# Optimization experiments

Hardware: AMD Instinct MI355X
Metric: run time of the kernel (lower is better)

## Reference

```python
import jax, jax.numpy as jnp
import numpy as np

N_NODES = 50000
N_EDGES = 800000
N_GRAPHS = 16
F_IN = 128
E_DIM = 16
HID = 32
HEADS = 2
EPS_BN = 1e-5


def gatv2_conv(x, edge_index, edge_attr, Wl, bl, Wr, br, We, att, bias, heads, out_ch):
    """PyG GATv2Conv (share_weights=False, concat=True, add_self_loops=True, fill_value='mean')."""
    n = x.shape[0]
    src, dst = edge_index[0], edge_index[1]
    loop = jnp.arange(n)
    src = jnp.concatenate([src, loop])
    dst = jnp.concatenate([dst, loop])
    ea = jnp.concatenate([edge_attr, jnp.broadcast_to(edge_attr.mean(0), (n, edge_attr.shape[1]))])
    x_l = (x @ Wl + bl).reshape(n, heads, out_ch)   # source transform
    x_r = (x @ Wr + br).reshape(n, heads, out_ch)   # target transform
    e = (ea @ We).reshape(-1, heads, out_ch)
    m = jax.nn.leaky_relu(x_l[src] + x_r[dst] + e, 0.2)      # [E, H, C]
    alpha = (m * att[None]).sum(-1)                          # [E, H]
    amax = jax.ops.segment_max(alpha, dst, num_segments=n)
    ex = jnp.exp(alpha - amax[dst])
    denom = jax.ops.segment_sum(ex, dst, num_segments=n)
    alpha = ex / (denom[dst] + 1e-16)
    out = jax.ops.segment_sum(x_l[src] * alpha[..., None], dst, num_segments=n)
    return out.reshape(n, heads * out_ch) + bias


def batch_norm(x, g, b):
    mu = x.mean(0)
    var = jnp.var(x, axis=0)  # biased, as torch BatchNorm1d training mode
    return (x - mu) * jax.lax.rsqrt(var + EPS_BN) * g + b


def setup_inputs() -> dict:
    key = jax.random.key(0)
    ks = jax.random.split(key, 24)
    s = 0.1
    d1 = HID * HEADS  # 64
    inp = {
        'x': jax.random.normal(ks[0], (N_NODES, F_IN), jnp.float32),
        'edge_index': jax.random.randint(ks[1], (2, N_EDGES), 0, N_NODES),
        'edge_attr': jax.random.normal(ks[2], (N_EDGES, E_DIM), jnp.float32),
        'batch': jnp.sort(jax.random.randint(ks[3], (N_NODES,), 0, N_GRAPHS)),
        'skip1_W': jax.random.normal(ks[4], (F_IN, d1)) * s,
        'skip1_b': jnp.zeros((d1,)),
        'conv1_Wl': jax.random.normal(ks[5], (F_IN, d1)) * s,
        'conv1_bl': jnp.zeros((d1,)),
        'conv1_Wr': jax.random.normal(ks[6], (F_IN, d1)) * s,
        'conv1_br': jnp.zeros((d1,)),
        'conv1_We': jax.random.normal(ks[7], (E_DIM, d1)) * s,
        'conv1_att': jax.random.normal(ks[8], (HEADS, HID)) * s,
        'conv1_bias': jnp.zeros((d1,)),
        'bn1_g': jnp.ones((d1,)),
        'bn1_b': jnp.zeros((d1,)),
        'skip2_W': jax.random.normal(ks[9], (d1, HID)) * s,
        'skip2_b': jnp.zeros((HID,)),
        'conv2_Wl': jax.random.normal(ks[10], (d1, HID)) * s,
        'conv2_bl': jnp.zeros((HID,)),
        'conv2_Wr': jax.random.normal(ks[11], (d1, HID)) * s,
        'conv2_br': jnp.zeros((HID,)),
        'conv2_We': jax.random.normal(ks[12], (E_DIM, HID)) * s,
        'conv2_att': jax.random.normal(ks[13], (1, HID)) * s,
        'conv2_bias': jnp.zeros((HID,)),
        'bn2_g': jnp.ones((HID,)),
        'bn2_b': jnp.zeros((HID,)),
    }
    return inp


def reference(x, edge_index, edge_attr, batch,
              skip1_W, skip1_b, conv1_Wl, conv1_bl, conv1_Wr, conv1_br, conv1_We, conv1_att, conv1_bias, bn1_g, bn1_b,
              skip2_W, skip2_b, conv2_Wl, conv2_bl, conv2_Wr, conv2_br, conv2_We, conv2_att, conv2_bias, bn2_g, bn2_b):
    h_proj = x @ skip1_W + skip1_b
    h = gatv2_conv(x, edge_index, edge_attr, conv1_Wl, conv1_bl, conv1_Wr, conv1_br, conv1_We, conv1_att, conv1_bias, HEADS, HID)
    h = jax.nn.elu(batch_norm(h, bn1_g, bn1_b) + h_proj)
    h_proj = h @ skip2_W + skip2_b
    h2 = gatv2_conv(h, edge_index, edge_attr, conv2_Wl, conv2_bl, conv2_Wr, conv2_br, conv2_We, conv2_att, conv2_bias, 1, HID)
    h2 = jax.nn.elu(batch_norm(h2, bn2_g, bn2_b) + h_proj)
    ones = jnp.ones((h2.shape[0],), h2.dtype)
    counts = jax.ops.segment_sum(ones, batch, num_segments=N_GRAPHS)
    x_mean = jax.ops.segment_sum(h2, batch, num_segments=N_GRAPHS) / jnp.maximum(counts, 1.0)[:, None]
    x_max = jax.ops.segment_max(h2, batch, num_segments=N_GRAPHS)
    x_max = jnp.where(counts[:, None] > 0, x_max, 0.0)
    return jnp.concatenate([x_mean, x_max], axis=1)
```

## Files before the change

kernel.cpp:

```cpp
#include <hip/hip_runtime.h>
#include <hip/hip_bf16.h>

#define NE 800000
#define NN 50000
#define NG 16
#define ETOT (NE + NN)

typedef unsigned short u16;
typedef __attribute__((ext_vector_type(8))) short short8;
typedef __attribute__((ext_vector_type(4))) float float4v;

__device__ __forceinline__ float b2f(u16 u) {
  return __uint_as_float(((unsigned)u) << 16);
}
__device__ __forceinline__ u16 f2b(float f) {
  __hip_bfloat16 b = __float2bfloat16(f);
  return *(u16*)&b;
}
__device__ __forceinline__ void cv8(uint4 v, float* o) {
  o[0] = __uint_as_float(v.x << 16);
  o[1] = __uint_as_float(v.x & 0xFFFF0000u);
  o[2] = __uint_as_float(v.y << 16);
  o[3] = __uint_as_float(v.y & 0xFFFF0000u);
  o[4] = __uint_as_float(v.z << 16);
  o[5] = __uint_as_float(v.z & 0xFFFF0000u);
  o[6] = __uint_as_float(v.w << 16);
  o[7] = __uint_as_float(v.w & 0xFFFF0000u);
}
__device__ __forceinline__ unsigned pk2(float a, float b) {
  return (unsigned)f2b(a) | ((unsigned)f2b(b) << 16);
}
__device__ __forceinline__ unsigned f2key(float f) {
  unsigned u = __float_as_uint(f);
  return (u & 0x80000000u) ? ~u : (u | 0x80000000u);
}
__device__ __forceinline__ float key2f(unsigned k) {
  unsigned u = (k & 0x80000000u) ? (k ^ 0x80000000u) : ~k;
  return __uint_as_float(u);
}
__device__ __forceinline__ int plaus(unsigned h) {
  unsigned eh = (h >> 7) & 0xFF;
  return (h == 0) || (eh >= 100 && eh <= 140);
}
__device__ __forceinline__ float lrelu(float v) {
  return (v > 0.f) ? v : 0.2f * v;
}

__global__ __launch_bounds__(256) void k_init(uint4* __restrict__ zbase, int zcnt16,
                                              const unsigned* __restrict__ a,
                                              const unsigned* __restrict__ b,
                                              const unsigned* __restrict__ c,
                                              int* __restrict__ flags) {
  uint4 z = {0, 0, 0, 0};
  for (int i = blockIdx.x * 256 + threadIdx.x; i < zcnt16; i += gridDim.x * 256)
    zbase[i] = z;
  if (blockIdx.x != 0) return;
  __shared__ int cnt[3];
  if (threadIdx.x < 3) cnt[threadIdx.x] = 0;
  __syncthreads();
  const unsigned* arr[3] = {a, b, c};
  for (int k = 0; k < 3; k++) {
    int ok = 0;
    for (int i = threadIdx.x; i < 4096; i += 256) {
      unsigned w = arr[k][i];
      ok += (plaus(w & 0xFFFFu) && plaus(w >> 16)) ? 1 : 0;
    }
    atomicAdd(&cnt[k], ok);
  }
  __syncthreads();
  if (threadIdx.x == 0) {
    int f0 = cnt[0] > 2048, f1 = cnt[1] > 2048, f2 = cnt[2] > 2048;
    flags[0] = f0;
    flags[1] = f1;
    flags[2] = f2;
    flags[3] = f0 && f1 && f2;
  }
}

__global__ __launch_bounds__(256) void k_histcol(const int* __restrict__ ei,
                                                 const void* __restrict__ ea,
                                                 const int* __restrict__ flg,
                                                 int* __restrict__ deg,
                                                 float* __restrict__ sums) {
  int gt = blockIdx.x * 256 + threadIdx.x;
  if (gt < ETOT) {
    int dst = (gt < NE) ? ei[NE + gt] : gt - NE;
    atomicAdd(&deg[dst], 1);
  }
  bool eb = flg[2] != 0;
  int col = gt & 15;
  int row = gt >> 4;
  int rstride = (gridDim.x * 256) >> 4;
  float s = 0.f;
  if (eb) {
    const u16* p = (const u16*)ea;
    for (int e = row; e < NE; e += rstride) s += b2f(p[(size_t)e * 16 + col]);
  } else {
    const float* p = (const float*)ea;
    for (int e = row; e < NE; e += rstride) s += p[(size_t)e * 16 + col];
  }
  __shared__ float ls[256];
  ls[threadIdx.x] = s;
  __syncthreads();
  if (threadIdx.x < 16) {
    float t = 0.f;
    for (int i = threadIdx.x; i < 256; i += 16) t += ls[i];
    atomicAdd(&sums[threadIdx.x], t);
  }
}

template <int K, int N>
__device__ __forceinline__ void load_W_f32(float* Wf, const void* W, bool wb) {
  if (wb) {
    const u16* Wp = (const u16*)W;
    for (int i = threadIdx.x; i < K * N / 8; i += 256) {
      float t[8];
      cv8(*(const uint4*)(Wp + i * 8), t);
#pragma unroll
      for (int q = 0; q < 8; q++) Wf[i * 8 + q] = t[q];
    }
  } else {
    const float* Wp = (const float*)W;
    for (int i = threadIdx.x; i < K * N / 4; i += 256) {
      float4 v = *(const float4*)(Wp + i * 4);
      Wf[i * 4 + 0] = v.x; Wf[i * 4 + 1] = v.y;
      Wf[i * 4 + 2] = v.z; Wf[i * 4 + 3] = v.w;
    }
  }
}

template <int K, int N, int RPB>
__device__ __forceinline__ void gemm_mfma_tile(
    const float* __restrict__ Wf,
    const void* __restrict__ xin, bool xb, bool wb,
    const void* __restrict__ bb, u16* __restrict__ out, int tile) {
  constexpr int CT = N / 16;
  constexpr int WPC = 4 / CT;
  constexpr int KK = K / 32;
  int lane = threadIdx.x & 63;
  int wave = threadIdx.x >> 6;
  int col = lane & 15;
  int quad = lane >> 4;
  int ct = wave % CT;
  int rt_off = wave / CT;
  short8 bh[KK], bl[KK];
#pragma unroll
  for (int kk = 0; kk < KK; kk++) {
    short8 th, tl;
#pragma unroll
    for (int j = 0; j < 8; j++) {
      float w = Wf[(kk * 32 + quad * 8 + j) * N + ct * 16 + col];
      u16 hb = f2b(w);
      th[j] = (short)hb;
      tl[j] = (short)f2b(w - b2f(hb));
    }
    bh[kk] = th;
    bl[kk] = tl;
  }
  float bias = wb ? b2f(((const u16*)bb)[ct * 16 + col])
                  : ((const float*)bb)[ct * 16 + col];
  int rt0 = tile * RPB;
  for (int i = rt_off; i < RPB; i += WPC) {
    int rt = rt0 + i;
    int row = rt * 16 + col;
    float4v acc = {0.f, 0.f, 0.f, 0.f};
    if (xb) {
      const u16* xp = (const u16*)xin;
#pragma unroll
      for (int kk = 0; kk < KK; kk++) {
        short8 af = *(const short8*)(xp + (size_t)row * K + kk * 32 + quad * 8);
        acc = __builtin_amdgcn_mfma_f32_16x16x32_bf16(af, bh[kk], acc, 0, 0, 0);
        if (!wb)
          acc = __builtin_amdgcn_mfma_f32_16x16x32_bf16(af, bl[kk], acc, 0, 0, 0);
      }
    } else {
      const float* xp = (const float*)xin;
#pragma unroll
      for (int kk = 0; kk < KK; kk++) {
        float4 v0 = *(const float4*)(xp + (size_t)row * K + kk * 32 + quad * 8);
        float4 v1 = *(const float4*)(xp + (size_t)row * K + kk * 32 + quad * 8 + 4);
        float a[8] = {v0.x, v0.y, v0.z, v0.w, v1.x, v1.y, v1.z, v1.w};
        short8 ah, al;
#pragma unroll
        for (int j = 0; j < 8; j++) {
          u16 hb = f2b(a[j]);
          ah[j] = (short)hb;
          al[j] = (short)f2b(a[j] - b2f(hb));
        }
        acc = __builtin_amdgcn_mfma_f32_16x16x32_bf16(ah, bh[kk], acc, 0, 0, 0);
        acc = __builtin_amdgcn_mfma_f32_16x16x32_bf16(al, bh[kk], acc, 0, 0, 0);
        if (!wb)
          acc = __builtin_amdgcn_mfma_f32_16x16x32_bf16(ah, bl[kk], acc, 0, 0, 0);
      }
    }
#pragma unroll
    for (int r = 0; r < 4; r++) {
      int orow = rt * 16 + quad * 4 + r;
      out[(size_t)orow * N + ct * 16 + col] = f2b(acc[r] + bias);
    }
  }
}

template <int K, int N, int TILES, int RPB>
__global__ __launch_bounds__(256) void k_scanlin1(
    const int* __restrict__ deg, int* __restrict__ start, int* __restrict__ cursor,
    const void* __restrict__ xin, const int* __restrict__ flg,
    const void* W0, const void* W1, const void* W2,
    const void* b0, const void* b1, const void* b2,
    u16* __restrict__ o0, u16* __restrict__ o1, u16* __restrict__ o2, int M) {
  (void)M;
  __shared__ __align__(16) float smem[K * N];

  if ((int)blockIdx.x == 3 * TILES) {
    int* wsum = (int*)smem;
    int t = threadIdx.x;
    int lane = t & 63;
    int wv = t >> 6;
    int carry = 0;
    for (int base = 0; base < NN; base += 1024) {
      int idx = base + t * 4;
      int4 d = {0, 0, 0, 0};
      if (idx + 3 < NN) {
        d = *(const int4*)(deg + idx);
      } else {
        if (idx + 0 < NN) d.x = deg[idx + 0];
        if (idx + 1 < NN) d.y = deg[idx + 1];
        if (idx + 2 < NN) d.z = deg[idx + 2];
        if (idx + 3 < NN) d.w = deg[idx + 3];
      }
      int s4 = d.x + d.y + d.z + d.w;
      int sc = s4;
#pragma unroll
      for (int ofs = 1; ofs < 64; ofs <<= 1) {
        int v = __shfl_up(sc, ofs, 64);
        if (lane >= ofs) sc += v;
      }
      if (lane == 63) wsum[wv] = sc;
      __syncthreads();
      int wbase = 0;
#pragma unroll
      for (int w = 0; w < 4; w++) {
        int ws = wsum[w];
        if (w < wv) wbase += ws;
      }
      int tile_total = wsum[0] + wsum[1] + wsum[2] + wsum[3];
      __syncthreads();
      int excl = carry + wbase + (sc - s4);
      int4 st;
      st.x = excl;
      st.y = excl + d.x;
      st.z = st.y + d.y;
      st.w = st.z + d.z;
      if (idx + 3 < NN) {
        *(int4*)(start + idx) = st;
        *(int4*)(cursor + idx) = st;
      } else {
        if (idx + 0 < NN) { start[idx + 0] = st.x; cursor[idx + 0] = st.x; }
        if (idx + 1 < NN) { start[idx + 1] = st.y; cursor[idx + 1] = st.y; }
        if (idx + 2 < NN) { start[idx + 2] = st.z; cursor[idx + 2] = st.z; }
        if (idx + 3 < NN) { start[idx + 3] = st.w; cursor[idx + 3] = st.w; }
      }
      carry += tile_total;
    }
    if (t == 0) start[NN] = carry;
    return;
  }
  int lidx = blockIdx.x;
  int wset = lidx / TILES;
  int tile = lidx % TILES;
  bool wb = flg[1] != 0;
  bool xb = flg[0] != 0;
  const void* W = wset == 0 ? W0 : (wset == 1 ? W1 : W2);
  const void* bb = wset == 0 ? b0 : (wset == 1 ? b1 : b2);
  u16* out = wset == 0 ? o0 : (wset == 1 ? o1 : o2);
  load_W_f32<K, N>(smem, W, wb);
  __syncthreads();
  gemm_mfma_tile<K, N, RPB>(smem, xin, xb, wb, bb, out, tile);
}

__global__ __launch_bounds__(256) void k_buildcsr_pay(
    const int* __restrict__ ei, const void* __restrict__ eattr,
    const int* __restrict__ flg, const float* __restrict__ mean_sums,
    int* __restrict__ cursor, int* __restrict__ csr_src,
    u16* __restrict__ ea16) {
  int e = blockIdx.x * 256 + threadIdx.x;
  if (e >= ETOT) return;
  bool eb = flg[2] != 0;
  int src, dst;
  if (e < NE) { src = ei[e]; dst = ei[NE + e]; } else { src = dst = e - NE; }
  float rec[16];
  if (e < NE) {
    if (eb) {
      const uint4* q = (const uint4*)((const u16*)eattr + (size_t)e * 16);
      cv8(q[0], rec);
      cv8(q[1], rec + 8);
    } else {
      const float* q = (const float*)eattr + (size_t)e * 16;
#pragma unroll
      for (int k = 0; k < 16; k++) rec[k] = q[k];
    }
  } else {
#pragma unroll
    for (int k = 0; k < 16; k++) rec[k] = mean_sums[k] * (1.0f / NE);
  }
  int pos = atomicAdd(&cursor[dst], 1);
  csr_src[pos] = src;
  u16 rb[16];
#pragma unroll
  for (int k = 0; k < 16; k++) rb[k] = f2b(rec[k]);
  uint4* dp = (uint4*)(ea16 + (size_t)pos * 16);
  dp[0] = *(uint4*)rb;
  dp[1] = *(uint4*)(rb + 8);
}

__global__ __launch_bounds__(256) void k_buildcsr(const int* __restrict__ ei,
                                                  int* __restrict__ cursor,
                                                  uint2* __restrict__ csr) {
  int e = blockIdx.x * 256 + threadIdx.x;
  if (e >= ETOT) return;
  int src, dst;
  if (e < NE) { src = ei[e]; dst = ei[NE + e]; } else { src = dst = e - NE; }
  int pos = atomicAdd(&cursor[dst], 1);
  uint2 r; r.x = (unsigned)src; r.y = (unsigned)e;
  csr[pos] = r;
}

template <int K, int N, int RPB>
__global__ __launch_bounds__(256) void k_lin3b(
    const void* __restrict__ xin, const int* __restrict__ flg,
    const void* W0, const void* W1, const void* W2,
    const void* b0, const void* b1, const void* b2,
    u16* __restrict__ o0, u16* __restrict__ o1, u16* __restrict__ o2, int M) {
  (void)M;
  __shared__ __align__(16) float smem[K * N];
  bool wb = flg[1] != 0;
  const void* W = blockIdx.y == 0 ? W0 : (blockIdx.y == 1 ? W1 : W2);
  const void* bb = blockIdx.y == 0 ? b0 : (blockIdx.y == 1 ? b1 : b2);
  u16* out = blockIdx.y == 0 ? o0 : (blockIdx.y == 1 ? o1 : o2);
  load_W_f32<K, N>(smem, W, wb);
  __syncthreads();
  gemm_mfma_tile<K, N, RPB>(smem, xin, true, wb, bb, out, blockIdx.x);
}

__device__ __forceinline__ float dot16b(const u16* __restrict__ p,
                                        const float* __restrict__ W) {
  float ea[16];
  const uint4* q = (const uint4*)p;
  cv8(q[0], ea);
  cv8(q[1], ea + 8);
  float s = 0.f;
#pragma unroll
  for (int k = 0; k < 16; k++) s += ea[k] * W[k];
  return s;
}
__device__ __forceinline__ float dot16u(const u16* __restrict__ p,
                                        const float* __restrict__ W) {
  const uint4* q = (const uint4*)p;
  uint4 A = q[0], B = q[1];
  unsigned w0 = (unsigned)__builtin_amdgcn_readfirstlane((int)A.x);
  unsigned w1 = (unsigned)__builtin_amdgcn_readfirstlane((int)A.y);
  unsigned w2 = (unsigned)__builtin_amdgcn_readfirstlane((int)A.z);
  unsigned w3 = (unsigned)__builtin_amdgcn_readfirstlane((int)A.w);
  unsigned w4 = (unsigned)__builtin_amdgcn_readfirstlane((int)B.x);
  unsigned w5 = (unsigned)__builtin_amdgcn_readfirstlane((int)B.y);
  unsigned w6 = (unsigned)__builtin_amdgcn_readfirstlane((int)B.z);
  unsigned w7 = (unsigned)__builtin_amdgcn_readfirstlane((int)B.w);
  float s = 0.f;
  s += __uint_as_float(w0 << 16) * W[0];
  s += __uint_as_float(w0 & 0xFFFF0000u) * W[1];
  s += __uint_as_float(w1 << 16) * W[2];
  s += __uint_as_float(w1 & 0xFFFF0000u) * W[3];
  s += __uint_as_float(w2 << 16) * W[4];
  s += __uint_as_float(w2 & 0xFFFF0000u) * W[5];
  s += __uint_as_float(w3 << 16) * W[6];
  s += __uint_as_float(w3 & 0xFFFF0000u) * W[7];
  s += __uint_as_float(w4 << 16) * W[8];
  s += __uint_as_float(w4 & 0xFFFF0000u) * W[9];
  s += __uint_as_float(w5 << 16) * W[10];
  s += __uint_as_float(w5 & 0xFFFF0000u) * W[11];
  s += __uint_as_float(w6 << 16) * W[12];
  s += __uint_as_float(w6 & 0xFFFF0000u) * W[13];
  s += __uint_as_float(w7 << 16) * W[14];
  s += __uint_as_float(w7 & 0xFFFF0000u) * W[15];
  return s;
}
__device__ __forceinline__ float dot16f(const float* __restrict__ q,
                                        const float* __restrict__ W) {
  float s = 0.f;
#pragma unroll
  for (int k = 0; k < 16; k++) s += q[k] * W[k];
  return s;
}

template <int H, int C>
__global__ __launch_bounds__(256) void k_fusedp(
    const int* __restrict__ start, const int* __restrict__ csr_src,
    const u16* __restrict__ pay, const int* __restrict__ flg,
    const u16* __restrict__ xl, const u16* __restrict__ xr,
    const void* We, const void* att, u16* __restrict__ agg) {
  constexpr int D = H * C;
  constexpr int NPW = 64 / D;
  bool wb = flg[1] != 0;
  int lane = threadIdx.x & 63;
  int ch = lane % D;
  float Wreg[16];
  if (wb) {
    const u16* Wp = (const u16*)We;
#pragma unroll
    for (int k = 0; k < 16; k++) Wreg[k] = b2f(Wp[k * D + ch]);
  } else {
    const float* Wp = (const float*)We;
#pragma unroll
    for (int k = 0; k < 16; k++) Wreg[k] = Wp[k * D + ch];
  }
  float attv = wb ? b2f(((const u16*)att)[ch]) : ((const float*)att)[ch];
  int wid = (blockIdx.x * 256 + threadIdx.x) >> 6;

  if constexpr (NPW == 1) {
    int node = __builtin_amdgcn_readfirstlane(wid);
    int s0 = __builtin_amdgcn_readfirstlane(start[node]);
    int s1 = __builtin_amdgcn_readfirstlane(start[node + 1]);
    float xrv = b2f(xr[(unsigned)node * D + ch]);
    float ssum = 0.f, acc = 0.f;
    int p = s0;
    for (; p + 3 < s1; p += 4) {
      int c0 = __builtin_amdgcn_readfirstlane(csr_src[p + 0]);
      int c1 = __builtin_amdgcn_readfirstlane(csr_src[p + 1]);
      int c2 = __builtin_amdgcn_readfirstlane(csr_src[p + 2]);
      int c3 = __builtin_amdgcn_readfirstlane(csr_src[p + 3]);
      float xlv0 = b2f(xl[(unsigned)c0 * D + ch]);
      float xlv1 = b2f(xl[(unsigned)c1 * D + ch]);
      float xlv2 = b2f(xl[(unsigned)c2 * D + ch]);
      float xlv3 = b2f(xl[(unsigned)c3 * D + ch]);
      float ev0 = dot16u(pay + (size_t)(p + 0) * 16, Wreg);
      float ev1 = dot16u(pay + (size_t)(p + 1) * 16, Wreg);
      float ev2 = dot16u(pay + (size_t)(p + 2) * 16, Wreg);
      float ev3 = dot16u(pay + (size_t)(p + 3) * 16, Wreg);
      float t0 = lrelu(xlv0 + xrv + ev0) * attv;
      float t1 = lrelu(xlv1 + xrv + ev1) * attv;
      float t2 = lrelu(xlv2 + xrv + ev2) * attv;
      float t3 = lrelu(xlv3 + xrv + ev3) * attv;
#pragma unroll
      for (int mk = 1; mk <= 16; mk <<= 1) {
        t0 += __shfl_xor(t0, mk, 64);
        t1 += __shfl_xor(t1, mk, 64);
        t2 += __shfl_xor(t2, mk, 64);
        t3 += __shfl_xor(t3, mk, 64);
      }
      float ex0 = __expf(t0);
      float ex1 = __expf(t1);
      float ex2 = __expf(t2);
      float ex3 = __expf(t3);
      ssum += (ex0 + ex1) + (ex2 + ex3);
      acc += ex0 * xlv0 + ex1 * xlv1;
      acc += ex2 * xlv2 + ex3 * xlv3;
    }
    for (; p < s1; ++p) {
      int c0 = __builtin_amdgcn_readfirstlane(csr_src[p]);
      float xlv = b2f(xl[(unsigned)c0 * D + ch]);
      float ev = dot16u(pay + (size_t)p * 16, Wreg);
      float t = lrelu(xlv + xrv + ev) * attv;
#pragma unroll
      for (int mk = 1; mk <= 16; mk <<= 1) t += __shfl_xor(t, mk, 64);
      float ex = __expf(t);
      ssum += ex;
      acc += ex * xlv;
    }
    agg[(size_t)node * D + ch] = f2b(acc / (ssum + 1e-16f));
  } else {
    int node = wid * NPW + lane / D;
    int s0 = start[node], s1 = start[node + 1];
    int deg = s1 - s0;
    int last = s1 - 1;
    int degmax = max(deg, __shfl_xor(deg, 32, 64));
    float xrv = b2f(xr[(unsigned)node * D + ch]);
    float ssum = 0.f, acc = 0.f;
    for (int i = 0; i < degmax; i += 4) {
      int p0 = min(s0 + i + 0, last);
      int p1 = min(s0 + i + 1, last);
      int p2 = min(s0 + i + 2, last);
      int p3 = min(s0 + i + 3, last);
      bool a0 = i + 0 < deg, a1 = i + 1 < deg, a2 = i + 2 < deg, a3 = i + 3 < deg;
      int c0 = csr_src[p0];
      int c1 = csr_src[p1];
      int c2 = csr_src[p2];
      int c3 = csr_src[p3];
      float xlv0 = b2f(xl[(unsigned)c0 * D + ch]);
      float xlv1 = b2f(xl[(unsigned)c1 * D + ch]);
      float xlv2 = b2f(xl[(unsigned)c2 * D + ch]);
      float xlv3 = b2f(xl[(unsigned)c3 * D + ch]);
      float ev0 = dot16b(pay + (size_t)p0 * 16, Wreg);
      float ev1 = dot16b(pay + (size_t)p1 * 16, Wreg);
      float ev2 = dot16b(pay + (size_t)p2 * 16, Wreg);
      float ev3 = dot16b(pay + (size_t)p3 * 16, Wreg);
      float t0 = lrelu(xlv0 + xrv + ev0) * attv;
      float t1 = lrelu(xlv1 + xrv + ev1) * attv;
      float t2 = lrelu(xlv2 + xrv + ev2) * attv;
      float t3 = lrelu(xlv3 + xrv + ev3) * attv;
#pragma unroll
      for (int mk = 1; mk <= 16; mk <<= 1) {
        t0 += __shfl_xor(t0, mk, 64);
        t1 += __shfl_xor(t1, mk, 64);
        t2 += __shfl_xor(t2, mk, 64);
        t3 += __shfl_xor(t3, mk, 64);
      }
      float ex0 = a0 ? __expf(t0) : 0.f;
      float ex1 = a1 ? __expf(t1) : 0.f;
      float ex2 = a2 ? __expf(t2) : 0.f;
      float ex3 = a3 ? __expf(t3) : 0.f;
      ssum += (ex0 + ex1) + (ex2 + ex3);
      acc += ex0 * xlv0 + ex1 * xlv1;
      acc += ex2 * xlv2 + ex3 * xlv3;
    }
    agg[(size_t)node * D + ch] = f2b(acc / (ssum + 1e-16f));
  }
}

template <int H, int C>
__global__ __launch_bounds__(256) void k_fusedg(
    const int* __restrict__ start, const uint2* __restrict__ csr,
    const void* __restrict__ eattr, const int* __restrict__ flg,
    const float* __restrict__ mean_sums,
    const u16* __restrict__ xl, const u16* __restrict__ xr,
    const void* We, const void* att, u16* __restrict__ agg) {
  constexpr int D = H * C;
  constexpr int NPW = 64 / D;
  bool wb = flg[1] != 0;
  bool eb = flg[2] != 0;
  int lane = threadIdx.x & 63;
  int ch = lane % D;
  float Wreg[16];
  if (wb) {
    const u16* Wp = (const u16*)We;
#pragma unroll
    for (int k = 0; k < 16; k++) Wreg[k] = b2f(Wp[k * D + ch]);
  } else {
    const float* Wp = (const float*)We;
#pragma unroll
    for (int k = 0; k < 16; k++) Wreg[k] = Wp[k * D + ch];
  }
  float attv = wb ? b2f(((const u16*)att)[ch]) : ((const float*)att)[ch];
  float ev_self = 0.f;
#pragma unroll
  for (int k = 0; k < 16; k++) ev_self += mean_sums[k] * (1.0f / NE) * Wreg[k];
  int wid = (blockIdx.x * 256 + threadIdx.x) >> 6;
  int node = wid * NPW + lane / D;
  int s0 = start[node], s1 = start[node + 1];
  int deg = s1 - s0;
  int last = s1 - 1;
  int degmax = deg;
  if constexpr (NPW == 2) degmax = max(deg, __shfl_xor(deg, 32, 64));
  float xrv = b2f(xr[(size_t)node * D + ch]);
  float ssum = 0.f, acc = 0.f;
  for (int i = 0; i < degmax; i += 2) {
    uint2 cr0 = csr[min(s0 + i, last)];
    uint2 cr1 = csr[min(s0 + i + 1, last)];
    bool a0 = i < deg, a1 = i + 1 < deg;
    float xlv0 = b2f(xl[(size_t)cr0.x * D + ch]);
    float xlv1 = b2f(xl[(size_t)cr1.x * D + ch]);
    float ev0 = cr0.y < NE ? (eb ? dot16b((const u16*)eattr + (size_t)cr0.y * 16, Wreg)
                                 : dot16f((const float*)eattr + (size_t)cr0.y * 16, Wreg))
                           : ev_self;
    float ev1 = cr1.y < NE ? (eb ? dot16b((const u16*)eattr + (size_t)cr1.y * 16, Wreg)
                                 : dot16f((const float*)eattr + (size_t)cr1.y * 16, Wreg))
                           : ev_self;
    float mv0 = xlv0 + xrv + ev0;
    float mv1 = xlv1 + xrv + ev1;
    mv0 = (mv0 > 0.f) ? mv0 : 0.2f * mv0;
    mv1 = (mv1 > 0.f) ? mv1 : 0.2f * mv1;
    float t0 = mv0 * attv, t1 = mv1 * attv;
#pragma unroll
    for (int mk = 1; mk <= 16; mk <<= 1) {
      t0 += __shfl_xor(t0, mk, 64);
      t1 += __shfl_xor(t1, mk, 64);
    }
    float ex0 = a0 ? __expf(t0) : 0.f;
    float ex1 = a1 ? __expf(t1) : 0.f;
    ssum += ex0 + ex1;
    acc += ex0 * xlv0 + ex1 * xlv1;
  }
  agg[(size_t)node * D + ch] = f2b(acc / (ssum + 1e-16f));
}

template <int D>
__global__ __launch_bounds__(256) void k_bnred(const u16* __restrict__ v,
                                               float* __restrict__ sum,
                                               float* __restrict__ sq, int M) {
  constexpr int RB = 256 / D;
  int tid = threadIdx.x;
  int c = tid % D;
  int rg = tid / D;
  float s = 0.f, q = 0.f;
  for (int r = blockIdx.x * RB + rg; r < M; r += gridDim.x * RB) {
    float x = b2f(v[(size_t)r * D + c]);
    s += x;
    q += x * x;
  }
  __shared__ float ls[256], lq[256];
  ls[tid] = s; lq[tid] = q;
  __syncthreads();
  if (tid < D) {
    float ts = 0.f, tq = 0.f;
    for (int i = tid; i < 256; i += D) { ts += ls[i]; tq += lq[i]; }
    atomicAdd(&sum[tid], ts);
    atomicAdd(&sq[tid], tq);
  }
}

template <int D>
__global__ __launch_bounds__(256) void k_bnapply(const u16* __restrict__ agg,
                                                 const u16* __restrict__ hp,
                                                 const float* __restrict__ sum,
                                                 const float* __restrict__ sq,
                                                 const void* g, const void* b,
                                                 const int* __restrict__ flg,
                                                 u16* __restrict__ out, int M) {
  bool wb = flg[1] != 0;
  int idx = blockIdx.x * 256 + threadIdx.x;
  if (idx >= M * D) return;
  int c = idx & (D - 1);
  float gc = wb ? b2f(((const u16*)g)[c]) : ((const float*)g)[c];
  float bc = wb ? b2f(((const u16*)b)[c]) : ((const float*)b)[c];
  float mu = sum[c] * (1.f / M);
  float var = fmaxf(sq[c] * (1.f / M) - mu * mu, 0.f);
  float sc = rsqrtf(var + 1e-5f) * gc;
  float v = (b2f(agg[idx]) - mu) * sc + bc + b2f(hp[idx]);
  v = v > 0.f ? v : expm1f(v);
  out[idx] = f2b(v);
}

__global__ __launch_bounds__(256) void k_poolall(
    const u16* __restrict__ agg2, const u16* __restrict__ hp2,
    const float* __restrict__ sum, const float* __restrict__ sq,
    const void* g, const void* b, const int* __restrict__ flg,
    const int* __restrict__ batch,
    float* __restrict__ pool_sum, unsigned* __restrict__ pool_maxk,
    float* __restrict__ pool_cnt, int* __restrict__ done_cnt,
    void* __restrict__ out) {
  bool wb = flg[1] != 0;
  int c = threadIdx.x & 31;
  int rg = threadIdx.x >> 5;
  float gc = wb ? b2f(((const u16*)g)[c]) : ((const float*)g)[c];
  float bc = wb ? b2f(((const u16*)b)[c]) : ((const float*)b)[c];
  float mu = sum[c] * (1.f / NN);
  float var = fmaxf(sq[c] * (1.f / NN) - mu * mu, 0.f);
  float scl = rsqrtf(var + 1e-5f) * gc;
  float sh = bc - mu * scl;

  const int NPB = 256;
  int n0 = blockIdx.x * NPB;
  int nend = min(n0 + NPB, NN);
  int cur = -1;
  float s = 0.f, mx = 0.f;
  int cnt = 0;
  for (int n = n0 + rg; n < nend; n += 8) {
    int gi = batch[n];
    float v = b2f(agg2[(size_t)n * 32 + c]) * scl + sh + b2f(hp2[(size_t)n * 32 + c]);
    v = v > 0.f ? v : expm1f(v);
    if (gi != cur) {
      if (cur >= 0) {
        atomicAdd(&pool_sum[cur * 32 + c], s);
        atomicMax(&pool_maxk[cur * 32 + c], f2key(mx));
        if (c == 0) atomicAdd(&pool_cnt[cur], (float)cnt);
      }
      cur = gi; s = 0.f; mx = -INFINITY; cnt = 0;
    }
    s += v;
    mx = fmaxf(mx, v);
    cnt++;
  }
  if (cur >= 0) {
    atomicAdd(&pool_sum[cur * 32 + c], s);
    atomicMax(&pool_maxk[cur * 32 + c], f2key(mx));
    if (c == 0) atomicAdd(&pool_cnt[cur], (float)cnt);
  }
  __threadfence();
  __syncthreads();
  __shared__ int lastblk;
  if (threadIdx.x == 0) lastblk = (atomicAdd(done_cnt, 1) == (int)gridDim.x - 1);
  __syncthreads();
  if (!lastblk) return;
  bool ob = flg[3] != 0;
  for (int idx = threadIdx.x; idx < NG * 64; idx += 256) {
    int gi = idx / 64, cc = idx % 64;
    float cntv = atomicAdd(&pool_cnt[gi], 0.f);
    float val;
    if (cc < 32) val = atomicAdd(&pool_sum[gi * 32 + cc], 0.f) / fmaxf(cntv, 1.f);
    else {
      unsigned k = atomicMax(&pool_maxk[gi * 32 + (cc - 32)], 0u);
      val = cntv > 0.f ? key2f(k) : 0.f;
    }
    if (ob) ((u16*)out)[idx] = f2b(val);
    else ((float*)out)[idx] = val;
  }
}

extern "C" void kernel_launch(void* const* d_in, const int* in_sizes, int n_in,
                              void* d_out, int out_size, void* d_ws, size_t ws_size,
                              hipStream_t stream) {
  (void)in_sizes; (void)n_in; (void)out_size;
  const void* x     = d_in[0];
  const int*  ei    = (const int*)d_in[1];
  const void* eattr = d_in[2];
  const int*  batch = (const int*)d_in[3];
  const void* skip1_W = d_in[4];
  const void* skip1_b = d_in[5];
  const void* c1_Wl = d_in[6];
  const void* c1_bl = d_in[7];
  const void* c1_Wr = d_in[8];
  const void* c1_br = d_in[9];
  const void* c1_We = d_in[10];
  const void* c1_att = d_in[11];
  const void* bn1_g = d_in[13];
  const void* bn1_b = d_in[14];
  const void* skip2_W = d_in[15];
  const void* skip2_b = d_in[16];
  const void* c2_Wl = d_in[17];
  const void* c2_bl = d_in[18];
  const void* c2_Wr = d_in[19];
  const void* c2_br = d_in[20];
  const void* c2_We = d_in[21];
  const void* c2_att = d_in[22];
  const void* bn2_g = d_in[24];
  const void* bn2_b = d_in[25];

  float* ws = (float*)d_ws;
  size_t off = 0;
  auto alloc = [&](size_t nfl) {
    float* p = ws + off;
    off += (nfl + 15) & ~(size_t)15;
    return p;
  };
  int*   flags      = (int*)alloc(16);
  float* mean_sums  = alloc(16);
  int*   deg        = (int*)alloc(NN);
  float* bnsum1     = alloc(64);
  float* bnsq1      = alloc(64);
  float* bnsum2     = alloc(32);
  float* bnsq2      = alloc(32);
  float* pool_cnt   = alloc(NG);
  float* pool_sum   = alloc(NG * 32);
  unsigned* pool_maxk = (unsigned*)alloc(NG * 32);
  int*   done_pool  = (int*)alloc(16);
  size_t zcnt16 = (off * sizeof(float)) / 16;
  size_t zoff = off;

  int* start   = (int*)alloc(NN + 1);
  int* cursor  = (int*)alloc(NN);
  int* csr_src = (int*)alloc(ETOT);
  u16* ea16    = (u16*)alloc((size_t)ETOT * 8);
  uint2* csr = nullptr;
  u16* xl1 = (u16*)alloc((size_t)NN * 32);
  u16* xr1 = (u16*)alloc((size_t)NN * 32);
  u16* hp1 = (u16*)alloc((size_t)NN * 32);
  u16* agg = (u16*)alloc((size_t)NN * 32);
  int tier3 = 0;
  if (off * sizeof(float) > ws_size) {
    tier3 = 1;
    off = zoff;
    start   = (int*)alloc(NN + 1);
    cursor  = (int*)alloc(NN);
    csr     = (uint2*)alloc((size_t)ETOT * 2);
    ea16    = nullptr;
    xl1 = (u16*)alloc((size_t)NN * 32);
    xr1 = (u16*)alloc((size_t)NN * 32);
    hp1 = (u16*)alloc((size_t)NN * 32);
    agg = (u16*)alloc((size_t)NN * 32);
  }
  u16* h1  = xr1;
  u16* xl2 = xl1;
  u16* xr2 = xl1 + (size_t)NN * 32;
  u16* hp2 = hp1;

  int eg = (ETOT + 255) / 256;

  k_init<<<128, 256, 0, stream>>>((uint4*)d_ws, (int)zcnt16,
                                  (const unsigned*)x, (const unsigned*)skip1_W,
                                  (const unsigned*)eattr, flags);
  k_histcol<<<eg, 256, 0, stream>>>(ei, eattr, flags, deg, mean_sums);
  k_scanlin1<128, 64, 625, 5><<<1876, 256, 0, stream>>>(
      deg, start, cursor, x, flags, c1_Wl, c1_Wr, skip1_W,
      c1_bl, c1_br, skip1_b, xl1, xr1, hp1, NN);
  if (!tier3) {
    k_buildcsr_pay<<<eg, 256, 0, stream>>>(ei, eattr, flags, mean_sums,
                                           cursor, csr_src, ea16);
  } else {
    k_buildcsr<<<eg, 256, 0, stream>>>(ei, cursor, csr);
  }
  if (!tier3) {
    k_fusedp<2, 32><<<NN / 4, 256, 0, stream>>>(start, csr_src, ea16, flags,
                                                xl1, xr1, c1_We, c1_att, agg);
  } else {
    k_fusedg<2, 32><<<NN / 4, 256, 0, stream>>>(start, csr, eattr, flags, mean_sums,
                                                xl1, xr1, c1_We, c1_att, agg);
  }
  k_bnred<64><<<256, 256, 0, stream>>>(agg, bnsum1, bnsq1, NN);
  k_bnapply<64><<<(NN * 64 + 255) / 256, 256, 0, stream>>>(agg, hp1, bnsum1, bnsq1,
                                                           bn1_g, bn1_b, flags, h1, NN);
  {
    dim3 g(625, 3);
    k_lin3b<64, 32, 5><<<g, 256, 0, stream>>>(h1, flags, c2_Wl, c2_Wr, skip2_W,
                                              c2_bl, c2_br, skip2_b,
                                              xl2, xr2, hp2, NN);
  }
  if (!tier3) {
    k_fusedp<1, 32><<<NN / 8, 256, 0, stream>>>(start, csr_src, ea16, flags,
                                                xl2, xr2, c2_We, c2_att, agg);
  } else {
    k_fusedg<1, 32><<<NN / 8, 256, 0, stream>>>(start, csr, eattr, flags, mean_sums,
                                                xl2, xr2, c2_We, c2_att, agg);
  }
  k_bnred<32><<<256, 256, 0, stream>>>(agg, bnsum2, bnsq2, NN);
  k_poolall<<<(NN + 255) / 256, 256, 0, stream>>>(agg, hp2, bnsum2, bnsq2,
                                                  bn2_g, bn2_b, flags, batch,
                                                  pool_sum, pool_maxk, pool_cnt,
                                                  done_pool, d_out);
}
```

Before: 574.3 us.

## Precompute edge-attribute projections with an MFMA GEMM before attention aggregation

Adds a kernel that computes edge_attr @ We for both layers over all CSR-ordered edges in one pass, using bf16 MFMA with a hi/lo weight split to keep precision. The attention kernels then read the precomputed per-edge, per-channel values instead of doing a 16-wide dot product per lane per edge. This trades ALU work in the gather loop for extra memory traffic: it writes and rereads about 850K×96 bf16 values. It also adds a workspace tier, falling back to the old path when the workspace is too small.

```diff
diff --git a/kernel.cpp b/kernel.cpp
--- a/kernel.cpp
+++ b/kernel.cpp
@@ -323,6 +323,75 @@
   int pos = atomicAdd(&cursor[dst], 1);
   uint2 r; r.x = (unsigned)src; r.y = (unsigned)e;
   csr[pos] = r;
+}
+
+__global__ __launch_bounds__(256) void k_ewgemm(
+    const u16* __restrict__ ea, const int* __restrict__ flg,
+    const void* We1, const void* We2,
+    u16* __restrict__ ew1, u16* __restrict__ ew2) {
+  bool wb = flg[1] != 0;
+  int lane = threadIdx.x & 63;
+  int col = lane & 15;
+  int quad = lane >> 4;
+  short8 b1h[4], b1l[4], b2h[2], b2l[2];
+#pragma unroll
+  for (int ct = 0; ct < 4; ct++) {
+    short8 th, tl;
+#pragma unroll
+    for (int j = 0; j < 8; j++) {
+      int k = quad * 8 + j;
+      float w = 0.f;
+      if (k < 16)
+        w = wb ? b2f(((const u16*)We1)[k * 64 + ct * 16 + col])
+               : ((const float*)We1)[k * 64 + ct * 16 + col];
+      u16 hb = f2b(w);
+      th[j] = (short)hb;
+      tl[j] = (short)f2b(w - b2f(hb));
+    }
+    b1h[ct] = th; b1l[ct] = tl;
+  }
+#pragma unroll
+  for (int ct = 0; ct < 2; ct++) {
+    short8 th, tl;
+#pragma unroll
+    for (int j = 0; j < 8; j++) {
+      int k = quad * 8 + j;
+      float w = 0.f;
+      if (k < 16)
+        w = wb ? b2f(((const u16*)We2)[k * 32 + ct * 16 + col])
+               : ((const float*)We2)[k * 32 + ct * 16 + col];
+      u16 hb = f2b(w);
+      th[j] = (short)hb;
+      tl[j] = (short)f2b(w - b2f(hb));
+    }
+    b2h[ct] = th; b2l[ct] = tl;
+  }
+  int nw = (gridDim.x * 256) >> 6;
+  int wid = (blockIdx.x * 256 + threadIdx.x) >> 6;
+  const int NT = ETOT / 16;
+  for (int rt = wid; rt < NT; rt += nw) {
+    int row = rt * 16 + col;
+    short8 af = {0, 0, 0, 0, 0, 0, 0, 0};
+    if (quad < 2) af = *(const short8*)(ea + (size_t)row * 16 + quad * 8);
+#pragma unroll
+    for (int ct = 0; ct < 4; ct++) {
+      float4v acc = {0.f, 0.f, 0.f, 0.f};
+      acc = __builtin_amdgcn_mfma_f32_16x16x32_bf16(af, b1h[ct], acc, 0, 0, 0);
+      acc = __builtin_amdgcn_mfma_f32_16x16x32_bf16(af, b1l[ct], acc, 0, 0, 0);
+#pragma unroll
+      for (int r = 0; r < 4; r++)
+        ew1[(size_t)(rt * 16 + quad * 4 + r) * 64 + ct * 16 + col] = f2b(acc[r]);
+    }
+#pragma unroll
+    for (int ct = 0; ct < 2; ct++) {
+      float4v acc = {0.f, 0.f, 0.f, 0.f};
+      acc = __builtin_amdgcn_mfma_f32_16x16x32_bf16(af, b2h[ct], acc, 0, 0, 0);
+      acc = __builtin_amdgcn_mfma_f32_16x16x32_bf16(af, b2l[ct], acc, 0, 0, 0);
+#pragma unroll
+      for (int r = 0; r < 4; r++)
+        ew2[(size_t)(rt * 16 + quad * 4 + r) * 32 + ct * 16 + col] = f2b(acc[r]);
+    }
+  }
 }
 
 template <int K, int N, int RPB>
@@ -392,10 +461,11 @@
   return s;
 }
 
-template <int H, int C>
+template <int H, int C, bool PRE>
 __global__ __launch_bounds__(256) void k_fusedp(
     const int* __restrict__ start, const int* __restrict__ csr_src,
-    const u16* __restrict__ pay, const int* __restrict__ flg,
+    const u16* __restrict__ pay, const u16* __restrict__ ewp,
+    const int* __restrict__ flg,
     const u16* __restrict__ xl, const u16* __restrict__ xr,
     const void* We, const void* att, u16* __restrict__ agg) {
   constexpr int D = H * C;
@@ -404,14 +474,16 @@
   int lane = threadIdx.x & 63;
   int ch = lane % D;
   float Wreg[16];
-  if (wb) {
-    const u16* Wp = (const u16*)We;
-#pragma unroll
-    for (int k = 0; k < 16; k++) Wreg[k] = b2f(Wp[k * D + ch]);
-  } else {
-    const float* Wp = (const float*)We;
-#pragma unroll
-    for (int k = 0; k < 16; k++) Wreg[k] = Wp[k * D + ch];
+  if constexpr (!PRE) {
+    if (wb) {
+      const u16* Wp = (const u16*)We;
+#pragma unroll
+      for (int k = 0; k < 16; k++) Wreg[k] = b2f(Wp[k * D + ch]);
+    } else {
+      const float* Wp = (const float*)We;
+#pragma unroll
+      for (int k = 0; k < 16; k++) Wreg[k] = Wp[k * D + ch];
+    }
   }
   float attv = wb ? b2f(((const u16*)att)[ch]) : ((const float*)att)[ch];
   int wid = (blockIdx.x * 256 + threadIdx.x) >> 6;
@@ -432,10 +504,18 @@
       float xlv1 = b2f(xl[(unsigned)c1 * D + ch]);
       float xlv2 = b2f(xl[(unsigned)c2 * D + ch]);
       float xlv3 = b2f(xl[(unsigned)c3 * D + ch]);
-      float ev0 = dot16u(pay + (size_t)(p + 0) * 16, Wreg);
-      float ev1 = dot16u(pay + (size_t)(p + 1) * 16, Wreg);
-      float ev2 = dot16u(pay + (size_t)(p + 2) * 16, Wreg);
-      float ev3 = dot16u(pay + (size_t)(p + 3) * 16, Wreg);
+      float ev0, ev1, ev2, ev3;
+      if constexpr (PRE) {
+        ev0 = b2f(ewp[(size_t)(p + 0) * D + ch]);
+        ev1 = b2f(ewp[(size_t)(p + 1) * D + ch]);
+        ev2 = b2f(ewp[(size_t)(p + 2) * D + ch]);
+        ev3 = b2f(ewp[(size_t)(p + 3) * D + ch]);
+      } else {
+        ev0 = dot16u(pay + (size_t)(p + 0) * 16, Wreg);
+        ev1 = dot16u(pay + (size_t)(p + 1) * 16, Wreg);
+        ev2 = dot16u(pay + (size_t)(p + 2) * 16, Wreg);
+        ev3 = dot16u(pay + (size_t)(p + 3) * 16, Wreg);
+      }
       float t0 = lrelu(xlv0 + xrv + ev0) * attv;
       float t1 = lrelu(xlv1 + xrv + ev1) * attv;
       float t2 = lrelu(xlv2 + xrv + ev2) * attv;
@@ -458,7 +538,9 @@
     for (; p < s1; ++p) {
       int c0 = __builtin_amdgcn_readfirstlane(csr_src[p]);
       float xlv = b2f(xl[(unsigned)c0 * D + ch]);
-      float ev = dot16u(pay + (size_t)p * 16, Wreg);
+      float ev;
+      if constexpr (PRE) ev = b2f(ewp[(size_t)p * D + ch]);
+      else ev = dot16u(pay + (size_t)p * 16, Wreg);
       float t = lrelu(xlv + xrv + ev) * attv;
 #pragma unroll
       for (int mk = 1; mk <= 16; mk <<= 1) t += __shfl_xor(t, mk, 64);
@@ -489,10 +571,18 @@
       float xlv1 = b2f(xl[(unsigned)c1 * D + ch]);
       float xlv2 = b2f(xl[(unsigned)c2 * D + ch]);
       float xlv3 = b2f(xl[(unsigned)c3 * D + ch]);
-      float ev0 = dot16b(pay + (size_t)p0 * 16, Wreg);
-      float ev1 = dot16b(pay + (size_t)p1 * 16, Wreg);
-      float ev2 = dot16b(pay + (size_t)p2 * 16, Wreg);
-      float ev3 = dot16b(pay + (size_t)p3 * 16, Wreg);
+      float ev0, ev1, ev2, ev3;
+      if constexpr (PRE) {
+        ev0 = b2f(ewp[(size_t)p0 * D + ch]);
+        ev1 = b2f(ewp[(size_t)p1 * D + ch]);
+        ev2 = b2f(ewp[(size_t)p2 * D + ch]);
+        ev3 = b2f(ewp[(size_t)p3 * D + ch]);
+      } else {
+        ev0 = dot16b(pay + (size_t)p0 * 16, Wreg);
+        ev1 = dot16b(pay + (size_t)p1 * 16, Wreg);
+        ev2 = dot16b(pay + (size_t)p2 * 16, Wreg);
+        ev3 = dot16b(pay + (size_t)p3 * 16, Wreg);
+      }
       float t0 = lrelu(xlv0 + xrv + ev0) * attv;
       float t1 = lrelu(xlv1 + xrv + ev1) * attv;
       float t2 = lrelu(xlv2 + xrv + ev2) * attv;
@@ -749,14 +839,29 @@
   int* cursor  = (int*)alloc(NN);
   int* csr_src = (int*)alloc(ETOT);
   u16* ea16    = (u16*)alloc((size_t)ETOT * 8);
+  u16* ew1     = (u16*)alloc((size_t)ETOT * 32);
+  u16* ew2     = (u16*)alloc((size_t)ETOT * 16);
   uint2* csr = nullptr;
   u16* xl1 = (u16*)alloc((size_t)NN * 32);
   u16* xr1 = (u16*)alloc((size_t)NN * 32);
   u16* hp1 = (u16*)alloc((size_t)NN * 32);
   u16* agg = (u16*)alloc((size_t)NN * 32);
-  int tier3 = 0;
+  int tier = 0;
   if (off * sizeof(float) > ws_size) {
-    tier3 = 1;
+    tier = 1;
+    off = zoff;
+    start   = (int*)alloc(NN + 1);
+    cursor  = (int*)alloc(NN);
+    csr_src = (int*)alloc(ETOT);
+    ea16    = (u16*)alloc((size_t)ETOT * 8);
+    ew1 = ew2 = nullptr;
+    xl1 = (u16*)alloc((size_t)NN * 32);
+    xr1 = (u16*)alloc((size_t)NN * 32);
+    hp1 = (u16*)alloc((size_t)NN * 32);
+    agg = (u16*)alloc((size_t)NN * 32);
+  }
+  if (tier == 1 && off * sizeof(float) > ws_size) {
+    tier = 2;
     off = zoff;
     start   = (int*)alloc(NN + 1);
     cursor  = (int*)alloc(NN);
@@ -781,15 +886,23 @@
   k_scanlin1<128, 64, 625, 5><<<1876, 256, 0, stream>>>(
       deg, start, cursor, x, flags, c1_Wl, c1_Wr, skip1_W,
       c1_bl, c1_br, skip1_b, xl1, xr1, hp1, NN);
-  if (!tier3) {
+  if (tier <= 1) {
     k_buildcsr_pay<<<eg, 256, 0, stream>>>(ei, eattr, flags, mean_sums,
                                            cursor, csr_src, ea16);
   } else {
     k_buildcsr<<<eg, 256, 0, stream>>>(ei, cursor, csr);
   }
-  if (!tier3) {
-    k_fusedp<2, 32><<<NN / 4, 256, 0, stream>>>(start, csr_src, ea16, flags,
-                                                xl1, xr1, c1_We, c1_att, agg);
+  if (tier == 0) {
+    k_ewgemm<<<1024, 256, 0, stream>>>(ea16, flags, c1_We, c2_We, ew1, ew2);
+  }
+  if (tier == 0) {
+    k_fusedp<2, 32, true><<<NN / 4, 256, 0, stream>>>(start, csr_src, ea16, ew1,
+                                                      flags, xl1, xr1, c1_We,
+                                                      c1_att, agg);
+  } else if (tier == 1) {
+    k_fusedp<2, 32, false><<<NN / 4, 256, 0, stream>>>(start, csr_src, ea16, nullptr,
+                                                       flags, xl1, xr1, c1_We,
+                                                       c1_att, agg);
   } else {
     k_fusedg<2, 32><<<NN / 4, 256, 0, stream>>>(start, csr, eattr, flags, mean_sums,
                                                 xl1, xr1, c1_We, c1_att, agg);
@@ -803,9 +916,14 @@
                                               c2_bl, c2_br, skip2_b,
                                               xl2, xr2, hp2, NN);
   }
-  if (!tier3) {
-    k_fusedp<1, 32><<<NN / 8, 256, 0, stream>>>(start, csr_src, ea16, flags,
-                                                xl2, xr2, c2_We, c2_att, agg);
+  if (tier == 0) {
+    k_fusedp<1, 32, true><<<NN / 8, 256, 0, stream>>>(start, csr_src, ea16, ew2,
+                                                      flags, xl2, xr2, c2_We,
+                                                      c2_att, agg);
+  } else if (tier == 1) {
+    k_fusedp<1, 32, false><<<NN / 8, 256, 0, stream>>>(start, csr_src, ea16, nullptr,
+                                                       flags, xl2, xr2, c2_We,
+                                                       c2_att, agg);
   } else {
     k_fusedg<1, 32><<<NN / 8, 256, 0, stream>>>(start, csr, eattr, flags, mean_sums,
                                                 xl2, xr2, c2_We, c2_att, agg);
```

Measured after the change: 574.0 us. No clear change (-0.1%).
